# Kernel tuning notes

Measured on AMD Instinct MI355X. Metric: run time of the kernel, lower is better.

Reference implementation:

```python
import jax, jax.numpy as jnp
import numpy as np
from jax import lax

B, CIN, COUT, K, L = 128, 8, 64, 33, 4096
STRIDE, PAD = 1, 16
HID, NW = 128, 3  # agent hidden, num wavelet types (morlet, mexhat, laplace)
MEXHAT_NORM = 2.0 / (np.sqrt(3.0) * np.pi ** 0.25)


def setup_inputs() -> dict:
    key = jax.random.key(0)
    ks = jax.random.split(key, 12)
    s = 0.05  # small init scale for agent weights
    return {
        "x": jax.random.normal(ks[0], (B, CIN, L), jnp.float32),
        # torch init: ones; add small noise so per-wavelet scales differ
        "superparams": jnp.ones((COUT, CIN, NW), jnp.float32)
        + 0.1 * jax.random.normal(ks[1], (COUT, CIN, NW), jnp.float32),
        "threshold": jnp.full((COUT,), 0.1, jnp.float32),
        "fw": s * jax.random.normal(ks[2], (2 * CIN, HID), jnp.float32),
        "fb": jnp.zeros((HID,), jnp.float32),
        "vw1": s * jax.random.normal(ks[3], (HID, HID), jnp.float32),
        "vb1": jnp.zeros((HID,), jnp.float32),
        "vw2": s * jax.random.normal(ks[4], (HID, 1), jnp.float32),
        "vb2": jnp.zeros((1,), jnp.float32),
        "aw1": s * jax.random.normal(ks[5], (HID, HID), jnp.float32),
        "ab1": jnp.zeros((HID,), jnp.float32),
        "aw2": s * jax.random.normal(ks[6], (HID, NW), jnp.float32),
        "ab2": jnp.zeros((NW,), jnp.float32),
    }


def _softplus_pos(p):
    return jax.nn.softplus(p) + 1e-6


def _make_kernels(superparams):
    # superparams: [COUT, CIN, NW] -> kernel bank [NW, COUT, CIN, K]
    grid = jnp.arange(-(K // 2), K // 2 + 1, dtype=jnp.float32)  # [K]
    scale = _softplus_pos(superparams)  # [COUT, CIN, NW]
    kernels = []
    for i, name in enumerate(("morlet", "mexhat", "laplace")):
        xi = grid[None, None, :] / scale[:, :, i : i + 1]  # [COUT, CIN, K]
        if name == "morlet":
            ker = jnp.exp(-0.5 * xi * xi) * jnp.cos(5.0 * xi)
        elif name == "mexhat":
            ker = MEXHAT_NORM * (1.0 - xi * xi) * jnp.exp(-0.5 * xi * xi)
        else:  # laplace
            ker = jnp.sign(grid)[None, None, :] * jnp.exp(-jnp.abs(xi))
        ker = ker - ker.mean(axis=-1, keepdims=True)
        ker = ker / (jnp.linalg.norm(ker, axis=-1, keepdims=True) + 1e-6)
        kernels.append(ker)
    return jnp.stack(kernels, axis=0)  # [NW, COUT, CIN, K]


def _q_values(states, fw, fb, vw1, vb1, vw2, vb2, aw1, ab1, aw2, ab2):
    h = jax.nn.relu(states @ fw + fb)                     # [B, HID]
    v = jax.nn.relu(h @ vw1 + vb1) @ vw2 + vb2            # [B, 1]
    a = jax.nn.relu(h @ aw1 + ab1) @ aw2 + ab2            # [B, NW]
    return v + a - a.mean(axis=1, keepdims=True)


def reference(x, superparams, threshold, fw, fb, vw1, vb1, vw2, vb2,
              aw1, ab1, aw2, ab2):
    # RL state: per-channel mean & (unbiased) std of the signal -> [B, 2*CIN]
    states = jnp.concatenate([x.mean(axis=-1), x.std(axis=-1, ddof=1)], axis=1)
    q = _q_values(states, fw, fb, vw1, vb1, vw2, vb2, aw1, ab1, aw2, ab2)
    actions = jnp.argmax(q, axis=1)                        # [B], greedy (eval)

    kernels = _make_kernels(superparams)                   # [NW, COUT, CIN, K]
    w_sel = kernels[actions]                               # [B, COUT, CIN, K]

    def conv_one(xb, wb):  # xb [CIN, L], wb [COUT, CIN, K]
        return lax.conv_general_dilated(
            xb[None], wb, window_strides=(STRIDE,), padding=[(PAD, PAD)],
            dimension_numbers=("NCH", "OIH", "NCH"))[0]

    y = jax.vmap(conv_one)(x, w_sel)                       # [B, COUT, Lout]

    # soft shrinkage (denoising) with strictly positive learnable threshold
    tau = _softplus_pos(threshold)[None, :, None]
    return jnp.sign(y) * jnp.maximum(jnp.abs(y) - tau, 0.0)
```

## Files before the change

kernel.cpp:

```cpp
#include <hip/hip_runtime.h>
#include <hip/hip_bf16.h>
#include <cmath>

#define B     128
#define CIN   8
#define COUT  64
#define K     33
#define KP    36
#define KKD   (KP * CIN)
#define NSL   (KKD / 32)
#define L     4096
#define PAD   16
#define HID   128
#define NW    3

#define TL    512
#define NROW  (TL + KP)

typedef __attribute__((ext_vector_type(8))) short short8;
typedef __attribute__((ext_vector_type(4))) float f32x4;

__device__ __forceinline__ float softplusf(float v) {
    return (v > 20.f) ? v : log1pf(expf(v));
}

__global__ __launch_bounds__(256) void prologue_kernel(
    const float* __restrict__ x,
    const float* __restrict__ fw, const float* __restrict__ fb,
    const float* __restrict__ aw1, const float* __restrict__ ab1,
    const float* __restrict__ aw2, const float* __restrict__ ab2,
    const float* __restrict__ sp,
    int* __restrict__ actions, __hip_bfloat16* __restrict__ bankbf)
{
    const int tid = threadIdx.x;

    if (blockIdx.x < B) {
        const int b = blockIdx.x;
        __shared__ float st[2 * CIN];
        __shared__ float h[HID];
        __shared__ float ha[HID];

        const int ci  = tid >> 5;
        const int sub = tid & 31;
        const float* xp = x + ((size_t)b * CIN + ci) * L;
        float s = 0.f, ss = 0.f;
        for (int j = sub; j < L / 4; j += 32) {
            float4 v = ((const float4*)xp)[j];
            s  += v.x + v.y + v.z + v.w;
            ss += v.x * v.x + v.y * v.y + v.z * v.z + v.w * v.w;
        }
        for (int m = 16; m; m >>= 1) {
            s  += __shfl_xor(s,  m);
            ss += __shfl_xor(ss, m);
        }
        if (sub == 0) {
            float mean = s / (float)L;
            float var  = fmaxf(ss - s * mean, 0.f) / (float)(L - 1);
            st[ci]       = mean;
            st[CIN + ci] = sqrtf(var);
        }
        __syncthreads();

        const int j = tid;
        if (j < HID) {
            float acc = fb[j];
            #pragma unroll
            for (int i = 0; i < 2 * CIN; ++i) acc = fmaf(st[i], fw[i * HID + j], acc);
            h[j] = fmaxf(acc, 0.f);
        }
        __syncthreads();
        if (j < HID) {
            float acc2 = ab1[j];
            for (int i = 0; i < HID; ++i) acc2 = fmaf(h[i], aw1[i * HID + j], acc2);
            ha[j] = fmaxf(acc2, 0.f);
        }
        __syncthreads();
        if (j == 0) {
            float best = -1e30f; int bi = 0;
            for (int w = 0; w < NW; ++w) {
                float a = ab2[w];
                for (int i = 0; i < HID; ++i) a = fmaf(ha[i], aw2[i * NW + w], a);
                if (a > best) { best = a; bi = w; }
            }
            actions[b] = bi;
        }
    } else {
        const int t = (blockIdx.x - B) * 256 + tid;
        if (t >= NW * COUT * CIN) return;
        const int nw = t >> 9;
        const int co = (t >> 3) & 63;
        const int ci = t & 7;

        const float p = sp[(co * CIN + ci) * NW + nw];
        const float scale = softplusf(p) + 1e-6f;

        float ker[K];
        float mean = 0.f;
        #pragma unroll
        for (int k = 0; k < K; ++k) {
            float g  = (float)(k - K / 2);
            float xi = g / scale;
            float v;
            if (nw == 0) {
                v = expf(-0.5f * xi * xi) * cosf(5.f * xi);
            } else if (nw == 1) {
                v = 0.8673250705840776f * (1.f - xi * xi) * expf(-0.5f * xi * xi);
            } else {
                float sgn = (g > 0.f) ? 1.f : ((g < 0.f) ? -1.f : 0.f);
                v = sgn * expf(-fabsf(xi));
            }
            ker[k] = v; mean += v;
        }
        mean *= (1.f / (float)K);
        float nrm = 0.f;
        #pragma unroll
        for (int k = 0; k < K; ++k) { ker[k] -= mean; nrm += ker[k] * ker[k]; }
        const float inv = 1.f / (sqrtf(nrm) + 1e-6f);

        __hip_bfloat16* dst = bankbf + ((size_t)(nw * COUT + co)) * KKD + ci;
        #pragma unroll
        for (int k = 0; k < K; ++k) dst[k * CIN] = __float2bfloat16(ker[k] * inv);
        #pragma unroll
        for (int k = K; k < KP; ++k) dst[k * CIN] = __float2bfloat16(0.f);
    }
}

__global__ __launch_bounds__(512, 4) void conv_kernel(
    const float* __restrict__ x, const __hip_bfloat16* __restrict__ bankbf,
    const int* __restrict__ actions, const float* __restrict__ threshold,
    float* __restrict__ out)
{
    const int cid = blockIdx.x;
    const int xcd = cid & 7;
    const int j2  = cid >> 3;
    const int b   = xcd + 8 * (j2 & 15);
    const int lx  = j2 >> 4;
    const int l0  = lx * TL;

    const int tid  = threadIdx.x;
    const int lane = tid & 63;
    const int w    = tid >> 6;
    const int p    = w & 1;
    const int q    = w >> 1;
    const int g    = lane >> 4;
    const int ln   = lane & 15;

    __shared__ short8 xT[NROW];

    {
        __hip_bfloat16* xb = (__hip_bfloat16*)xT;
        for (int idx = tid; idx < CIN * NROW; idx += 512) {
            int ci = idx / NROW;
            int r  = idx - ci * NROW;
            int gp = l0 - PAD + r;
            float f = (gp >= 0 && gp < L) ? x[((size_t)b * CIN + ci) * L + gp] : 0.f;
            xb[r * CIN + ci] = __float2bfloat16(f);
        }
    }

    const int act = __builtin_amdgcn_readfirstlane(actions[b]);
    const short8* wq = (const short8*)(bankbf + (size_t)act * COUT * KKD);
    short8 aQ[2][NSL];
    #pragma unroll
    for (int cc = 0; cc < 2; ++cc) {
        const short8* wrow = wq + ((2 * p + cc) * 16 + ln) * (KKD / 8);
        #pragma unroll
        for (int s = 0; s < NSL; ++s) aQ[cc][s] = wrow[4 * s + g];
    }

    float tau[2];
    #pragma unroll
    for (int cc = 0; cc < 2; ++cc)
        tau[cc] = softplusf(threshold[(2 * p + cc) * 16 + ln]) + 1e-6f;

    __syncthreads();

    const int wl0 = q * (TL / 4);
    #pragma unroll
    for (int lt = 0; lt < 4; ++lt) {
        const int lbase = wl0 + lt * 32;
        const int r0    = lbase + ln + g;
        f32x4 acc[2][2] = {{{0.f,0.f,0.f,0.f},{0.f,0.f,0.f,0.f}},
                           {{0.f,0.f,0.f,0.f},{0.f,0.f,0.f,0.f}}};
        #pragma unroll
        for (int s = 0; s < NSL; ++s) {
            short8 bf0 = xT[r0 + 4 * s];
            short8 bf1 = xT[r0 + 16 + 4 * s];
            acc[0][0] = __builtin_amdgcn_mfma_f32_16x16x32_bf16(bf0, aQ[0][s], acc[0][0], 0, 0, 0);
            acc[1][0] = __builtin_amdgcn_mfma_f32_16x16x32_bf16(bf0, aQ[1][s], acc[1][0], 0, 0, 0);
            acc[0][1] = __builtin_amdgcn_mfma_f32_16x16x32_bf16(bf1, aQ[0][s], acc[0][1], 0, 0, 0);
            acc[1][1] = __builtin_amdgcn_mfma_f32_16x16x32_bf16(bf1, aQ[1][s], acc[1][1], 0, 0, 0);
        }
        #pragma unroll
        for (int cc = 0; cc < 2; ++cc) {
            const int co = (2 * p + cc) * 16 + ln;
            float* orow = &out[((size_t)b * COUT + co) * L + l0 + lbase + 4 * g];
            #pragma unroll
            for (int sub = 0; sub < 2; ++sub) {
                f32x4 a = acc[cc][sub];
                f32x4 o;
                o[0] = copysignf(fmaxf(fabsf(a[0]) - tau[cc], 0.f), a[0]);
                o[1] = copysignf(fmaxf(fabsf(a[1]) - tau[cc], 0.f), a[1]);
                o[2] = copysignf(fmaxf(fabsf(a[2]) - tau[cc], 0.f), a[2]);
                o[3] = copysignf(fmaxf(fabsf(a[3]) - tau[cc], 0.f), a[3]);
                __builtin_nontemporal_store(o, (f32x4*)(orow + 16 * sub));
            }
        }
    }
}

extern "C" void kernel_launch(void* const* d_in, const int* in_sizes, int n_in,
                              void* d_out, int out_size, void* d_ws, size_t ws_size,
                              hipStream_t stream)
{
    const float* x           = (const float*)d_in[0];
    const float* superparams = (const float*)d_in[1];
    const float* threshold   = (const float*)d_in[2];
    const float* fw          = (const float*)d_in[3];
    const float* fb          = (const float*)d_in[4];
    const float* aw1         = (const float*)d_in[9];
    const float* ab1         = (const float*)d_in[10];
    const float* aw2         = (const float*)d_in[11];
    const float* ab2         = (const float*)d_in[12];
    float* out = (float*)d_out;

    int* actions            = (int*)d_ws;
    __hip_bfloat16* bankbf  = (__hip_bfloat16*)((char*)d_ws + 1024);

    prologue_kernel<<<B + 6, 256, 0, stream>>>(
        x, fw, fb, aw1, ab1, aw2, ab2, superparams, actions, bankbf);
    conv_kernel<<<B * (L / TL), 512, 0, stream>>>(
        x, bankbf, actions, threshold, out);
}
```

Before: 231.4 us.

## Stage conv outputs through LDS for coalesced stores, double tile length, vectorize input load

Each wave now writes its shrunk MFMA results into a per-wave LDS buffer and reads them back so every lane stores a contiguous 128-byte row segment per output channel, replacing the scattered 16-byte nontemporal stores. The L tile grows to 1024, halving the block count, and the input halo load switches to float4 global reads. The grid becomes 2D, dropping the XCD-aware block-to-batch mapping. This adds LDS traffic, about 40KB of extra shared memory per block that may lower occupancy, and plain instead of nontemporal stores.

After: 197.9 us. 14.5% less time.

```diff
diff --git a/kernel.cpp b/kernel.cpp
--- a/kernel.cpp
+++ b/kernel.cpp
@@ -14,8 +14,9 @@
 #define HID   128
 #define NW    3
 
-#define TL    512
+#define TL    1024
 #define NROW  (TL + KP)
+#define OSTR  40
 
 typedef __attribute__((ext_vector_type(8))) short short8;
 typedef __attribute__((ext_vector_type(4))) float f32x4;
@@ -130,13 +131,8 @@
     const int* __restrict__ actions, const float* __restrict__ threshold,
     float* __restrict__ out)
 {
-    const int cid = blockIdx.x;
-    const int xcd = cid & 7;
-    const int j2  = cid >> 3;
-    const int b   = xcd + 8 * (j2 & 15);
-    const int lx  = j2 >> 4;
-    const int l0  = lx * TL;
-
+    const int b  = blockIdx.y;
+    const int l0 = blockIdx.x * TL;
     const int tid  = threadIdx.x;
     const int lane = tid & 63;
     const int w    = tid >> 6;
@@ -146,15 +142,29 @@
     const int ln   = lane & 15;
 
     __shared__ short8 xT[NROW];
+    __shared__ float  obuf[8][32 * OSTR];
 
     {
         __hip_bfloat16* xb = (__hip_bfloat16*)xT;
-        for (int idx = tid; idx < CIN * NROW; idx += 512) {
-            int ci = idx / NROW;
-            int r  = idx - ci * NROW;
-            int gp = l0 - PAD + r;
-            float f = (gp >= 0 && gp < L) ? x[((size_t)b * CIN + ci) * L + gp] : 0.f;
-            xb[r * CIN + ci] = __float2bfloat16(f);
+        for (int idx = tid; idx < CIN * (NROW / 4); idx += 512) {
+            int ci = idx / (NROW / 4);
+            int r4 = (idx - ci * (NROW / 4)) * 4;
+            int gp = l0 - PAD + r4;
+            const float* xp = x + ((size_t)b * CIN + ci) * L;
+            if (gp >= 0 && gp <= L - 4) {
+                float4 v = *(const float4*)&xp[gp];
+                xb[(r4 + 0) * CIN + ci] = __float2bfloat16(v.x);
+                xb[(r4 + 1) * CIN + ci] = __float2bfloat16(v.y);
+                xb[(r4 + 2) * CIN + ci] = __float2bfloat16(v.z);
+                xb[(r4 + 3) * CIN + ci] = __float2bfloat16(v.w);
+            } else {
+                #pragma unroll
+                for (int e = 0; e < 4; ++e) {
+                    int gpe = gp + e;
+                    float f = (gpe >= 0 && gpe < L) ? xp[gpe] : 0.f;
+                    xb[(r4 + e) * CIN + ci] = __float2bfloat16(f);
+                }
+            }
         }
     }
 
@@ -173,11 +183,13 @@
     for (int cc = 0; cc < 2; ++cc)
         tau[cc] = softplusf(threshold[(2 * p + cc) * 16 + ln]) + 1e-6f;
 
+    const int co_r = lane >> 3;
+    const int lc   = lane & 7;
+
     __syncthreads();
 
     const int wl0 = q * (TL / 4);
-    #pragma unroll
-    for (int lt = 0; lt < 4; ++lt) {
+    for (int lt = 0; lt < (TL / 4) / 32; ++lt) {
         const int lbase = wl0 + lt * 32;
         const int r0    = lbase + ln + g;
         f32x4 acc[2][2] = {{{0.f,0.f,0.f,0.f},{0.f,0.f,0.f,0.f}},
@@ -191,10 +203,9 @@
             acc[0][1] = __builtin_amdgcn_mfma_f32_16x16x32_bf16(bf1, aQ[0][s], acc[0][1], 0, 0, 0);
             acc[1][1] = __builtin_amdgcn_mfma_f32_16x16x32_bf16(bf1, aQ[1][s], acc[1][1], 0, 0, 0);
         }
+
         #pragma unroll
         for (int cc = 0; cc < 2; ++cc) {
-            const int co = (2 * p + cc) * 16 + ln;
-            float* orow = &out[((size_t)b * COUT + co) * L + l0 + lbase + 4 * g];
             #pragma unroll
             for (int sub = 0; sub < 2; ++sub) {
                 f32x4 a = acc[cc][sub];
@@ -203,8 +214,16 @@
                 o[1] = copysignf(fmaxf(fabsf(a[1]) - tau[cc], 0.f), a[1]);
                 o[2] = copysignf(fmaxf(fabsf(a[2]) - tau[cc], 0.f), a[2]);
                 o[3] = copysignf(fmaxf(fabsf(a[3]) - tau[cc], 0.f), a[3]);
-                __builtin_nontemporal_store(o, (f32x4*)(orow + 16 * sub));
-            }
+                *(f32x4*)&obuf[w][(cc * 16 + ln) * OSTR + 16 * sub + 4 * g] = o;
+            }
+        }
+
+        #pragma unroll
+        for (int i = 0; i < 4; ++i) {
+            const int col = co_r + 8 * i;
+            f32x4 v = *(const f32x4*)&obuf[w][col * OSTR + 4 * lc];
+            const int co = (2 * p + (col >> 4)) * 16 + (col & 15);
+            *(f32x4*)&out[((size_t)b * COUT + co) * L + l0 + lbase + 4 * lc] = v;
         }
     }
 }
@@ -229,6 +248,6 @@
 
     prologue_kernel<<<B + 6, 256, 0, stream>>>(
         x, fw, fb, aw1, ab1, aw2, ab2, superparams, actions, bankbf);
-    conv_kernel<<<B * (L / TL), 512, 0, stream>>>(
+    conv_kernel<<<dim3(L / TL, B), 512, 0, stream>>>(
         x, bankbf, actions, threshold, out);
 }
```
